# Optimization experiments

Hardware: AMD Instinct MI355X
Metric: run time of the kernel (lower is better)

## Reference

```python
import jax, jax.numpy as jnp
import numpy as np

HEAD_DIM = 64  # scale = head_dim ** -0.5


def setup_inputs() -> dict:
    key = jax.random.key(0)
    ks = jax.random.split(key, 5)
    B, S, E = 8, 8192, 1024
    L, D = 64, 256          # n_latent_vec, latent_dim
    H = HEAD_DIM
    return {
        "input_tensor": jax.random.normal(ks[0], (B, S, E), dtype=jnp.float32),
        "latents": jax.random.normal(ks[1], (L, D), dtype=jnp.float32),
        "Wq": jax.random.normal(ks[2], (H, D), dtype=jnp.float32) * (1.0 / np.sqrt(D)),
        "Wk": jax.random.normal(ks[3], (H, E), dtype=jnp.float32) * (1.0 / np.sqrt(E)),
        "Wv": jax.random.normal(ks[4], (H, E), dtype=jnp.float32) * (1.0 / np.sqrt(E)),
    }


def reference(input_tensor, latents, Wq, Wk, Wv):
    # non-cached path, seq_len == max_seq_len so no truncation
    # queries: broadcast shared latents over batch -> [B, L, H]
    q = jnp.einsum('ld,hd->lh', latents, Wq)                 # [L, H]
    k = jnp.einsum('bse,he->bsh', input_tensor, Wk)           # [B, S, H]
    v = jnp.einsum('bse,he->bsh', input_tensor, Wv)           # [B, S, H]
    scale = HEAD_DIM ** -0.5
    scores = jnp.einsum('lh,bsh->bls', q, k) * scale          # [B, L, S]
    weights = jax.nn.softmax(scores, axis=-1)                 # dropout is identity (p=0 / eval)
    out = jnp.einsum('bls,bsh->blh', weights, v)              # [B, L, H]
    return out
```

## Files before the change

### kernel.cpp

```cpp
#include <hip/hip_runtime.h>
#include <stdint.h>


typedef __attribute__((__ext_vector_type__(4))) float f32x4;
typedef __attribute__((__ext_vector_type__(8))) short bf16x8;

__device__ __forceinline__ unsigned short f2bf(float f) {
    union { float f; uint32_t u; } v; v.f = f;
    uint32_t u = v.u;
    return (unsigned short)((u + 0x7fffu + ((u >> 16) & 1u)) >> 16);
}

__device__ __forceinline__ unsigned long long pack4(f32x4 v) {
    return (unsigned long long)f2bf(v[0])        |
           ((unsigned long long)f2bf(v[1]) << 16) |
           ((unsigned long long)f2bf(v[2]) << 32) |
           ((unsigned long long)f2bf(v[3]) << 48);
}

__global__ __launch_bounds__(256) void prep_kernel(
    const float* __restrict__ latents, const float* __restrict__ Wq,
    const float* __restrict__ Wk, const float* __restrict__ Wv,
    unsigned short* __restrict__ wkv, unsigned short* __restrict__ qbf)
{
    const int blk = blockIdx.x, tid = threadIdx.x;
    if (blk < 128) {
        const float* src = (blk < 64) ? (Wk + (size_t)blk * 1024)
                                      : (Wv + (size_t)(blk - 64) * 1024);
        for (int i = tid; i < 1024; i += 256)
            wkv[(size_t)blk * 1024 + i] = f2bf(src[i]);
    } else {
        const int l = (blk - 128) * 4 + (tid >> 6);
        const int h = tid & 63;
        float a = 0.f;
        #pragma unroll 8
        for (int d = 0; d < 256; ++d)
            a += latents[l * 256 + d] * Wq[h * 256 + d];
        qbf[l * 64 + h] = f2bf(a * 0.125f);
    }
}

__global__ __launch_bounds__(256) void fused_kernel(
    const float* __restrict__ x, const unsigned short* __restrict__ wkv,
    const unsigned short* __restrict__ qbf,
    float* __restrict__ Opart, float* __restrict__ mpart, float* __restrict__ spart)
{
    __shared__ unsigned short smem[36864];
    unsigned short* Ab = smem;
    unsigned short* Bb = smem + 18432;
    unsigned short* Cs = smem;
    unsigned short* Ps = smem + 17408;
    unsigned short* qs = smem + 26112;
    __shared__ float red[4][64];
    __shared__ float Mrow[64];

    const int tid = threadIdx.x;
    const int wave = tid >> 6, lane = tid & 63;
    const int g = lane >> 4, c = lane & 15;
    const int wr = wave >> 1, wc = wave & 1;
    const size_t r0 = (size_t)blockIdx.x * 128;

    const int rowS = tid >> 1, hS = tid & 1;

    f32x4 acc[4][4];
    #pragma unroll
    for (int i = 0; i < 4; ++i)
        #pragma unroll
        for (int j = 0; j < 4; ++j)
            acc[i][j] = f32x4{0.f, 0.f, 0.f, 0.f};

    f32x4 areg[8];
    uint4  breg[4];

    #pragma unroll
    for (int j = 0; j < 8; ++j)
        areg[j] = *(const f32x4*)(x + (r0 + rowS) * 1024 + 4 * hS + 8 * j);
    #pragma unroll
    for (int j = 0; j < 4; ++j)
        breg[j] = *(const uint4*)(wkv + (size_t)rowS * 1024 + 8 * hS + 16 * j);
    #pragma unroll
    for (int j = 0; j < 8; ++j)
        *(unsigned long long*)&Ab[rowS * 72 + 4 * hS + 8 * j] = pack4(areg[j]);
    #pragma unroll
    for (int j = 0; j < 4; ++j)
        *(uint4*)&Bb[rowS * 72 + 8 * hS + 16 * j] = breg[j];
    __syncthreads();

    for (int t = 0; t < 16; ++t) {
        const int buf = t & 1;
        if (t < 15) {
            const int e0 = (t + 1) * 64;
            #pragma unroll
            for (int j = 0; j < 8; ++j)
                areg[j] = *(const f32x4*)(x + (r0 + rowS) * 1024 + e0 + 4 * hS + 8 * j);
            #pragma unroll
            for (int j = 0; j < 4; ++j)
                breg[j] = *(const uint4*)(wkv + (size_t)rowS * 1024 + e0 + 8 * hS + 16 * j);
        }
        #pragma unroll
        for (int k0 = 0; k0 < 2; ++k0) {
            bf16x8 af[4], bfr[4];
            #pragma unroll
            for (int ml = 0; ml < 4; ++ml)
                af[ml] = *(const bf16x8*)&Ab[(buf * 128 + 64 * wr + 16 * ml + c) * 72
                                             + 32 * k0 + 8 * g];
            #pragma unroll
            for (int nc = 0; nc < 4; ++nc)
                bfr[nc] = *(const bf16x8*)&Bb[(buf * 128 + 64 * wc + 16 * nc + c) * 72
                                              + 32 * k0 + 8 * g];
            #pragma unroll
            for (int ml = 0; ml < 4; ++ml)
                #pragma unroll
                for (int nc = 0; nc < 4; ++nc)
                    acc[ml][nc] = __builtin_amdgcn_mfma_f32_16x16x32_bf16(
                        af[ml], bfr[nc], acc[ml][nc], 0, 0, 0);
        }
        if (t < 15) {
            const int nb = buf ^ 1;
            #pragma unroll
            for (int j = 0; j < 8; ++j)
                *(unsigned long long*)&Ab[(nb * 128 + rowS) * 72 + 4 * hS + 8 * j] =
                    pack4(areg[j]);
            #pragma unroll
            for (int j = 0; j < 4; ++j)
                *(uint4*)&Bb[(nb * 128 + rowS) * 72 + 8 * hS + 16 * j] = breg[j];
        }
        __syncthreads();
    }

    #pragma unroll
    for (int ml = 0; ml < 4; ++ml)
        #pragma unroll
        for (int nc = 0; nc < 4; ++nc)
            #pragma unroll
            for (int r = 0; r < 4; ++r)
                Cs[(64 * wr + 16 * ml + 4 * g + r) * 136 + 64 * wc + 16 * nc + c] =
                    f2bf(acc[ml][nc][r]);
    {
        const int rowQ = tid >> 2, colQ = (tid & 3) * 8;
        #pragma unroll
        for (int j = 0; j < 2; ++j)
            *(uint4*)&qs[rowQ * 72 + colQ + 32 * j] =
                *(const uint4*)(qbf + rowQ * 64 + colQ + 32 * j);
    }
    __syncthreads();

    f32x4 sc[4][2];
    #pragma unroll
    for (int ml = 0; ml < 4; ++ml)
        #pragma unroll
        for (int ns = 0; ns < 2; ++ns)
            sc[ml][ns] = f32x4{0.f, 0.f, 0.f, 0.f};
    #pragma unroll
    for (int k0 = 0; k0 < 2; ++k0) {
        bf16x8 aq[4];
        #pragma unroll
        for (int ml = 0; ml < 4; ++ml)
            aq[ml] = *(const bf16x8*)&qs[(16 * ml + c) * 72 + 32 * k0 + 8 * g];
        #pragma unroll
        for (int ns = 0; ns < 2; ++ns) {
            bf16x8 bk = *(const bf16x8*)&Cs[(32 * wave + 16 * ns + c) * 136 + 32 * k0 + 8 * g];
            #pragma unroll
            for (int ml = 0; ml < 4; ++ml)
                sc[ml][ns] = __builtin_amdgcn_mfma_f32_16x16x32_bf16(
                    aq[ml], bk, sc[ml][ns], 0, 0, 0);
        }
    }

    float mloc[4][4];
    #pragma unroll
    for (int ml = 0; ml < 4; ++ml)
        #pragma unroll
        for (int r = 0; r < 4; ++r)
            mloc[ml][r] = fmaxf(sc[ml][0][r], sc[ml][1][r]);
    #pragma unroll
    for (int off = 1; off <= 8; off <<= 1)
        #pragma unroll
        for (int ml = 0; ml < 4; ++ml)
            #pragma unroll
            for (int r = 0; r < 4; ++r)
                mloc[ml][r] = fmaxf(mloc[ml][r], __shfl_xor(mloc[ml][r], off));
    if (c == 0)
        #pragma unroll
        for (int ml = 0; ml < 4; ++ml)
            #pragma unroll
            for (int r = 0; r < 4; ++r)
                red[wave][16 * ml + 4 * g + r] = mloc[ml][r];
    __syncthreads();
    if (tid < 64) {
        float m = red[0][tid];
        m = fmaxf(m, red[1][tid]); m = fmaxf(m, red[2][tid]); m = fmaxf(m, red[3][tid]);
        Mrow[tid] = m;
    }
    __syncthreads();

    float ssum[4][4];
    #pragma unroll
    for (int ml = 0; ml < 4; ++ml)
        #pragma unroll
        for (int r = 0; r < 4; ++r)
            ssum[ml][r] = 0.f;
    #pragma unroll
    for (int ml = 0; ml < 4; ++ml)
        #pragma unroll
        for (int r = 0; r < 4; ++r) {
            const int l = 16 * ml + 4 * g + r;
            const float mr = Mrow[l];
            #pragma unroll
            for (int ns = 0; ns < 2; ++ns) {
                float p = __expf(sc[ml][ns][r] - mr);
                unsigned short pb = f2bf(p);
                Ps[l * 136 + 32 * wave + 16 * ns + c] = pb;
                union { uint32_t u; float f; } pv; pv.u = (uint32_t)pb << 16;
                ssum[ml][r] += pv.f;
            }
        }
    #pragma unroll
    for (int off = 1; off <= 8; off <<= 1)
        #pragma unroll
        for (int ml = 0; ml < 4; ++ml)
            #pragma unroll
            for (int r = 0; r < 4; ++r)
                ssum[ml][r] += __shfl_xor(ssum[ml][r], off);
    if (c == 0)
        #pragma unroll
        for (int ml = 0; ml < 4; ++ml)
            #pragma unroll
            for (int r = 0; r < 4; ++r)
                red[wave][16 * ml + 4 * g + r] = ssum[ml][r];
    __syncthreads();
    if (tid < 64) {
        const float s = red[0][tid] + red[1][tid] + red[2][tid] + red[3][tid];
        mpart[(size_t)blockIdx.x * 64 + tid] = Mrow[tid];
        spart[(size_t)blockIdx.x * 64 + tid] = s;
    }

    f32x4 o[4];
    #pragma unroll
    for (int nh = 0; nh < 4; ++nh) o[nh] = f32x4{0.f, 0.f, 0.f, 0.f};
    #pragma unroll
    for (int ks = 0; ks < 4; ++ks) {
        bf16x8 ap = *(const bf16x8*)&Ps[(16 * wave + c) * 136 + 32 * ks + 8 * g];
        #pragma unroll
        for (int nh = 0; nh < 4; ++nh) {
            bf16x8 bv;
            #pragma unroll
            for (int j = 0; j < 8; ++j)
                bv[j] = (short)Cs[(32 * ks + 8 * g + j) * 136 + 64 + 16 * nh + c];
            o[nh] = __builtin_amdgcn_mfma_f32_16x16x32_bf16(ap, bv, o[nh], 0, 0, 0);
        }
    }
    const size_t pb = (size_t)blockIdx.x * 64;
    #pragma unroll
    for (int nh = 0; nh < 4; ++nh)
        #pragma unroll
        for (int r = 0; r < 4; ++r) {
            const int l = 16 * wave + 4 * g + r;
            const int h = 16 * nh + c;
            Opart[(pb + l) * 64 + h] = o[nh][r];
        }
}

__global__ __launch_bounds__(64) void combine_kernel(
    const float* __restrict__ Opart, const float* __restrict__ mpart,
    const float* __restrict__ spart, float* __restrict__ out)
{
    const int b = blockIdx.x >> 6, l = blockIdx.x & 63, h = threadIdx.x;
    float M = -3.0e38f;
    #pragma unroll 8
    for (int ch = 0; ch < 64; ++ch)
        M = fmaxf(M, mpart[((size_t)(b * 64 + ch)) * 64 + l]);
    float den = 0.f, acc = 0.f;
    #pragma unroll 8
    for (int ch = 0; ch < 64; ++ch) {
        const size_t idx = ((size_t)(b * 64 + ch)) * 64 + l;
        const float w = __expf(mpart[idx] - M);
        den += w * spart[idx];
        acc += w * Opart[idx * 64 + h];
    }
    out[((size_t)blockIdx.x) * 64 + h] = acc / den;
}

extern "C" void kernel_launch(void* const* d_in, const int* in_sizes, int n_in,
                              void* d_out, int out_size, void* d_ws, size_t ws_size,
                              hipStream_t stream)
{
    const float* x       = (const float*)d_in[0];
    const float* latents = (const float*)d_in[1];
    const float* Wq      = (const float*)d_in[2];
    const float* Wk      = (const float*)d_in[3];
    const float* Wv      = (const float*)d_in[4];
    float* out = (float*)d_out;
    char* ws = (char*)d_ws;

    unsigned short* wkv = (unsigned short*)(ws);
    unsigned short* qbf = (unsigned short*)(ws + 262144);
    float* Opart = (float*)(ws + 270336);
    float* mpart = (float*)(ws + 270336 + 8388608);
    float* spart = (float*)(ws + 270336 + 8388608 + 131072);

    hipLaunchKernelGGL(prep_kernel, dim3(144), dim3(256), 0, stream,
                       latents, Wq, Wk, Wv, wkv, qbf);
    hipLaunchKernelGGL(fused_kernel, dim3(512), dim3(256), 0, stream,
                       x, wkv, qbf, Opart, mpart, spart);
    hipLaunchKernelGGL(combine_kernel, dim3(512), dim3(64), 0, stream,
                       Opart, mpart, spart, out);
}
```

Measured before the change: 93.49 us.

## Stream K/V GEMM tiles via direct global-to-LDS loads with XOR swizzle

Replaces the register-staged loads of the x and wkv tiles, which converted x to bf16 before storing it to LDS, with global_load_lds DMA copies into XOR-swizzled LDS buffers. x is now kept in fp32 in LDS and converted to bf16 when fragments are read. The K step per stage is halved to 32, so there are twice as many iterations and barriers. Launch bounds now request 2 blocks per CU. This aims to cut VGPR pressure and load/convert/store overhead and to overlap better, at the cost of double the LDS footprint for A, repeated conversion work per wave, and more synchronisation.

```diff
diff --git a/kernel.cpp b/kernel.cpp
--- a/kernel.cpp
+++ b/kernel.cpp
@@ -16,6 +16,12 @@
            ((unsigned long long)f2bf(v[1]) << 16) |
            ((unsigned long long)f2bf(v[2]) << 32) |
            ((unsigned long long)f2bf(v[3]) << 48);
+}
+
+__device__ __forceinline__ void gld_lds16(const void* g, void* l) {
+    __builtin_amdgcn_global_load_lds(
+        (const __attribute__((address_space(1))) unsigned int*)g,
+        (__attribute__((address_space(3))) unsigned int*)l, 16, 0, 0);
 }
 
 __global__ __launch_bounds__(256) void prep_kernel(
@@ -40,17 +46,17 @@
     }
 }
 
-__global__ __launch_bounds__(256) void fused_kernel(
+__global__ __launch_bounds__(256, 2) void fused_kernel(
     const float* __restrict__ x, const unsigned short* __restrict__ wkv,
     const unsigned short* __restrict__ qbf,
     float* __restrict__ Opart, float* __restrict__ mpart, float* __restrict__ spart)
 {
-    __shared__ unsigned short smem[36864];
-    unsigned short* Ab = smem;
-    unsigned short* Bb = smem + 18432;
-    unsigned short* Cs = smem;
-    unsigned short* Ps = smem + 17408;
-    unsigned short* qs = smem + 26112;
+    __shared__ __align__(16) unsigned char smem[61440];
+    float* Af          = (float*)smem;
+    unsigned short* Bb = (unsigned short*)(smem + 32768);
+    unsigned short* Cs = (unsigned short*)smem;
+    unsigned short* qs = (unsigned short*)(smem + 34816);
+    unsigned short* Ps = (unsigned short*)(smem + 44032);
     __shared__ float red[4][64];
     __shared__ float Mrow[64];
 
@@ -60,7 +66,13 @@
     const int wr = wave >> 1, wc = wave & 1;
     const size_t r0 = (size_t)blockIdx.x * 128;
 
-    const int rowS = tid >> 1, hS = tid & 1;
+    const int arow = lane >> 3;
+    const int agr  = (lane & 7) ^ arow;
+    const int brow = lane >> 2;
+    const int bgr  = (lane & 3) ^ (brow & 3) ^ ((brow >> 2) & 3);
+
+    const float* aSrc = x + (r0 + 8 * wave + arow) * 1024 + 4 * agr;
+    const unsigned short* bSrc = wkv + (size_t)(16 * wave + brow) * 1024 + 8 * bgr;
 
     f32x4 acc[4][4];
     #pragma unroll
@@ -69,62 +81,48 @@
         for (int j = 0; j < 4; ++j)
             acc[i][j] = f32x4{0.f, 0.f, 0.f, 0.f};
 
-    f32x4 areg[8];
-    uint4  breg[4];
-
-    #pragma unroll
-    for (int j = 0; j < 8; ++j)
-        areg[j] = *(const f32x4*)(x + (r0 + rowS) * 1024 + 4 * hS + 8 * j);
     #pragma unroll
     for (int j = 0; j < 4; ++j)
-        breg[j] = *(const uint4*)(wkv + (size_t)rowS * 1024 + 8 * hS + 16 * j);
-    #pragma unroll
-    for (int j = 0; j < 8; ++j)
-        *(unsigned long long*)&Ab[rowS * 72 + 4 * hS + 8 * j] = pack4(areg[j]);
-    #pragma unroll
-    for (int j = 0; j < 4; ++j)
-        *(uint4*)&Bb[rowS * 72 + 8 * hS + 16 * j] = breg[j];
-    __syncthreads();
-
-    for (int t = 0; t < 16; ++t) {
+        gld_lds16(aSrc + (size_t)j * 32 * 1024, Af + (32 * j + 8 * wave) * 32);
+    #pragma unroll
+    for (int j = 0; j < 2; ++j)
+        gld_lds16(bSrc + (size_t)j * 64 * 1024, Bb + (64 * j + 16 * wave) * 32);
+    __syncthreads();
+
+    for (int t = 0; t < 32; ++t) {
         const int buf = t & 1;
-        if (t < 15) {
-            const int e0 = (t + 1) * 64;
-            #pragma unroll
-            for (int j = 0; j < 8; ++j)
-                areg[j] = *(const f32x4*)(x + (r0 + rowS) * 1024 + e0 + 4 * hS + 8 * j);
+        if (t < 31) {
+            const int e0 = (t + 1) * 32;
+            const int nb = buf ^ 1;
             #pragma unroll
             for (int j = 0; j < 4; ++j)
-                breg[j] = *(const uint4*)(wkv + (size_t)rowS * 1024 + e0 + 8 * hS + 16 * j);
-        }
-        #pragma unroll
-        for (int k0 = 0; k0 < 2; ++k0) {
-            bf16x8 af[4], bfr[4];
-            #pragma unroll
-            for (int ml = 0; ml < 4; ++ml)
-                af[ml] = *(const bf16x8*)&Ab[(buf * 128 + 64 * wr + 16 * ml + c) * 72
-                                             + 32 * k0 + 8 * g];
+                gld_lds16(aSrc + (size_t)j * 32 * 1024 + e0,
+                          Af + (nb * 128 + 32 * j + 8 * wave) * 32);
+            #pragma unroll
+            for (int j = 0; j < 2; ++j)
+                gld_lds16(bSrc + (size_t)j * 64 * 1024 + e0,
+                          Bb + (nb * 128 + 64 * j + 16 * wave) * 32);
+        }
+        bf16x8 af[4], bfr[4];
+        #pragma unroll
+        for (int ml = 0; ml < 4; ++ml) {
+            const float* base = Af + (buf * 128 + 64 * wr + 16 * ml + c) * 32;
+            f32x4 u = *(const f32x4*)(base + 4 * ((2 * g)     ^ (c & 7)));
+            f32x4 v = *(const f32x4*)(base + 4 * ((2 * g + 1) ^ (c & 7)));
+            union { unsigned long long q[2]; bf16x8 b; } w;
+            w.q[0] = pack4(u); w.q[1] = pack4(v);
+            af[ml] = w.b;
+        }
+        #pragma unroll
+        for (int nc = 0; nc < 4; ++nc)
+            bfr[nc] = *(const bf16x8*)(Bb + (buf * 128 + 64 * wc + 16 * nc + c) * 32
+                                       + 8 * (g ^ (c & 3) ^ ((c >> 2) & 3)));
+        #pragma unroll
+        for (int ml = 0; ml < 4; ++ml)
             #pragma unroll
             for (int nc = 0; nc < 4; ++nc)
-                bfr[nc] = *(const bf16x8*)&Bb[(buf * 128 + 64 * wc + 16 * nc + c) * 72
-                                              + 32 * k0 + 8 * g];
-            #pragma unroll
-            for (int ml = 0; ml < 4; ++ml)
-                #pragma unroll
-                for (int nc = 0; nc < 4; ++nc)
-                    acc[ml][nc] = __builtin_amdgcn_mfma_f32_16x16x32_bf16(
-                        af[ml], bfr[nc], acc[ml][nc], 0, 0, 0);
-        }
-        if (t < 15) {
-            const int nb = buf ^ 1;
-            #pragma unroll
-            for (int j = 0; j < 8; ++j)
-                *(unsigned long long*)&Ab[(nb * 128 + rowS) * 72 + 4 * hS + 8 * j] =
-                    pack4(areg[j]);
-            #pragma unroll
-            for (int j = 0; j < 4; ++j)
-                *(uint4*)&Bb[(nb * 128 + rowS) * 72 + 8 * hS + 16 * j] = breg[j];
-        }
+                acc[ml][nc] = __builtin_amdgcn_mfma_f32_16x16x32_bf16(
+                    af[ml], bfr[nc], acc[ml][nc], 0, 0, 0);
         __syncthreads();
     }
 
```

Result: faster. 85.97 us (-8.0%).
